# Performance work log

Hardware: AMD Instinct MI355X
Metric: run time of the kernel (lower is better)

Reference implementation:

```python
import jax, jax.numpy as jnp
import numpy as np

B, S, D, H, DFF, L = 32, 512, 512, 8, 2048, 3
DK = D // H
NEG = -1e32


def _ln(x, g, b):
    m = jnp.mean(x, axis=-1, keepdims=True)
    v = jnp.mean((x - m) ** 2, axis=-1, keepdims=True)
    return (x - m) / jnp.sqrt(v + 1e-5) * g + b


def _mha(query, key, value, mask, zero_pad, gam, Wk, bk, Wv, bv, Wo, bo):
    # kq_same: q and k both use k_linear
    q = (query @ Wk + bk).reshape(B, S, H, DK).transpose(0, 2, 1, 3)
    k = (key @ Wk + bk).reshape(B, S, H, DK).transpose(0, 2, 1, 3)
    v = (value @ Wv + bv).reshape(B, S, H, DK).transpose(0, 2, 1, 3)
    scores = jnp.einsum('bhid,bhjd->bhij', q, k) / jnp.sqrt(jnp.float32(DK))
    # distance-decay rescoring (no-grad in original)
    p = jax.nn.softmax(jnp.where(mask, scores, NEG), axis=-1) * mask
    distcum = jnp.cumsum(p, axis=-1)
    disttotal = jnp.sum(p, axis=-1, keepdims=True)
    idx = jnp.arange(S)
    pos = jnp.abs(idx[None, :] - idx[:, None]).astype(jnp.float32)  # [S,S]
    dist = jax.lax.stop_gradient(
        jnp.sqrt(jnp.clip((disttotal - distcum) * pos[None, None], 0.0, None)))
    gamma = -jax.nn.softplus(gam)[None, :, None, None]  # [1,H,1,1]
    total_effect = jnp.clip(jnp.exp(dist * gamma), 1e-5, 1e5)
    scores = jnp.where(mask, scores * total_effect, NEG)
    scores = jax.nn.softmax(scores, axis=-1)
    if zero_pad:
        scores = scores * (idx[:, None] > 0)[None, None, :, :].astype(scores.dtype) * 0 + \
                 scores * (idx > 0).astype(scores.dtype)[None, None, :, None]
    out = jnp.einsum('bhij,bhjd->bhid', scores, v)
    out = out.transpose(0, 2, 1, 3).reshape(B, S, D)
    return out @ Wo + bo


def _layer(i, mask, zero_pad, query, key, values, apply_pos,
           Wk, bk, Wv, bv, Wo, bo, gammas, ln1_g, ln1_b, W1, b1, W2, b2, ln2_g, ln2_b):
    a = _mha(query, key, values, mask, zero_pad, gammas[i],
             Wk[i], bk[i], Wv[i], bv[i], Wo[i], bo[i])
    x = _ln(query + a, ln1_g[i], ln1_b[i])
    if apply_pos:
        f = jax.nn.relu(x @ W1[i] + b1[i]) @ W2[i] + b2[i]
        x = _ln(x + f, ln2_g[i], ln2_b[i])
    return x


def setup_inputs() -> dict:
    key = jax.random.key(0)
    ks = jax.random.split(key, 12)
    sc = 0.02
    inp = {
        'q_embed_data': jax.random.normal(ks[0], (B, S, D), jnp.float32),
        'qa_embed_data': jax.random.normal(ks[1], (B, S, D), jnp.float32),
        'Wk': jax.random.normal(ks[2], (L, D, D), jnp.float32) * sc,
        'bk': jnp.zeros((L, D), jnp.float32),
        'Wv': jax.random.normal(ks[3], (L, D, D), jnp.float32) * sc,
        'bv': jnp.zeros((L, D), jnp.float32),
        'Wo': jax.random.normal(ks[4], (L, D, D), jnp.float32) * sc,
        'bo': jnp.zeros((L, D), jnp.float32),
        'gammas': jax.random.normal(ks[5], (L, H), jnp.float32) * 0.5,
        'ln1_g': jnp.ones((L, D), jnp.float32),
        'ln1_b': jnp.zeros((L, D), jnp.float32),
        'W1': jax.random.normal(ks[6], (L, D, DFF), jnp.float32) * sc,
        'b1': jnp.zeros((L, DFF), jnp.float32),
        'W2': jax.random.normal(ks[7], (L, DFF, D), jnp.float32) * sc,
        'b2': jnp.zeros((L, D), jnp.float32),
        'ln2_g': jnp.ones((L, D), jnp.float32),
        'ln2_b': jnp.zeros((L, D), jnp.float32),
    }
    return inp


def reference(q_embed_data, qa_embed_data, Wk, bk, Wv, bv, Wo, bo, gammas,
              ln1_g, ln1_b, W1, b1, W2, b2, ln2_g, ln2_b):
    P = (Wk, bk, Wv, bv, Wo, bo, gammas, ln1_g, ln1_b, W1, b1, W2, b2, ln2_g, ln2_b)
    mask1 = jnp.tril(jnp.ones((S, S), bool), 0)[None, None]   # peek current+past
    mask0 = jnp.tril(jnp.ones((S, S), bool), -1)[None, None]  # peek only past
    y = qa_embed_data
    x = q_embed_data
    # blocks_1 (n_blocks=1): mask=1, self-attn, apply_pos
    y = _layer(0, mask1, False, y, y, y, True, *P)
    # blocks_2 (2 layers): first mask=1 no FFN, second mask=0 zero_pad cross-attn to y
    x = _layer(1, mask1, False, x, x, x, False, *P)
    x = _layer(2, mask0, True, x, x, y, True, *P)
    return x
```

## Files before the change

kernel.cpp:

```cpp
#include <hip/hip_runtime.h>

#define BB   32
#define SS   512
#define DDIM 512
#define HH   8
#define DFFN 2048
#define MR   (BB*SS)

typedef unsigned int   u32;
typedef unsigned short u16;
typedef unsigned char  u8;
typedef __attribute__((ext_vector_type(8))) short bf16x8;
typedef __attribute__((ext_vector_type(4))) float f32x4;

__device__ __forceinline__ u32 packbf2(float x, float y) {
  u32 ux = __float_as_uint(x), uy = __float_as_uint(y);
  u32 hx = (ux + 0x7FFFu + ((ux >> 16) & 1u)) >> 16;
  u32 hy = (uy + 0x7FFFu + ((uy >> 16) & 1u)) >> 16;
  return hx | (hy << 16);
}
__device__ __forceinline__ u16 pack1bf(float x) {
  u32 u = __float_as_uint(x);
  return (u16)((u + 0x7FFFu + ((u >> 16) & 1u)) >> 16);
}
__device__ __forceinline__ float bf1(u16 h)  { return __uint_as_float(((u32)h) << 16); }

__device__ __forceinline__ float redsum2(float v) {
  v += __shfl_xor(v, 16, 64);
  v += __shfl_xor(v, 32, 64);
  return v;
}
__device__ __forceinline__ float redmax2(float v) {
  v = fmaxf(v, __shfl_xor(v, 16, 64));
  v = fmaxf(v, __shfl_xor(v, 32, 64));
  return v;
}

__global__ __launch_bounds__(256) void pack_flat(const float* __restrict__ in,
                                                 u16* __restrict__ out) {
  size_t i = ((size_t)blockIdx.x * 256 + threadIdx.x) * 8;
  float4 a = *(const float4*)(in + i);
  float4 b = *(const float4*)(in + i + 4);
  uint4 o;
  o.x = packbf2(a.x, a.y); o.y = packbf2(a.z, a.w);
  o.z = packbf2(b.x, b.y); o.w = packbf2(b.z, b.w);
  *(uint4*)(out + i) = o;
}

__global__ __launch_bounds__(256) void pack_w_t(const float* __restrict__ in,
                                                u16* __restrict__ out, int K, int N) {
  __shared__ float tile[64][65];
  const int t  = threadIdx.x;
  const int n0 = blockIdx.x * 64, k0 = blockIdx.y * 64;
  in  += (size_t)blockIdx.z * K * N;
  out += (size_t)blockIdx.z * N * K;
  #pragma unroll
  for (int it = 0; it < 4; ++it) {
    int idx = it * 256 + t;
    int kk = idx >> 4, n4 = idx & 15;
    float4 v = *(const float4*)(in + (size_t)(k0 + kk) * N + n0 + n4 * 4);
    tile[kk][n4*4+0] = v.x; tile[kk][n4*4+1] = v.y;
    tile[kk][n4*4+2] = v.z; tile[kk][n4*4+3] = v.w;
  }
  __syncthreads();
  #pragma unroll
  for (int it = 0; it < 4; ++it) {
    int idx = it * 256 + t;
    int nn = idx >> 4, g = idx & 15;
    uint2 o;
    o.x = packbf2(tile[g*4+0][nn], tile[g*4+1][nn]);
    o.y = packbf2(tile[g*4+2][nn], tile[g*4+3][nn]);
    *(uint2*)(out + (size_t)(n0 + nn) * K + k0 + g * 4) = o;
  }
}

__global__ __launch_bounds__(512, 2) void gemm8(
    const u16* __restrict__ Aa, const u16* __restrict__ Ab, int lda,
    const u16* __restrict__ Ba, const u16* __restrict__ Bb, int ldb,
    const float* __restrict__ biasa, const float* __restrict__ biasb,
    float* __restrict__ outFa, float* __restrict__ outFb,
    u16* __restrict__ outBa, u16* __restrict__ outBb,
    int ldc, int Kz, int relu)
{
  __shared__ __align__(16) u8 lds[131072];

  const int z = blockIdx.z;
  const u16* A    = z ? Ab : Aa;
  const u16* Bt   = z ? Bb : Ba;
  const float* bias = z ? biasb : biasa;
  float* outF = z ? outFb : outFa;
  u16*   outB = z ? outBb : outBa;

  const int nwg  = gridDim.x * gridDim.y;
  const int orig = blockIdx.y * gridDim.x + blockIdx.x;
  const int q8   = nwg >> 3, r8 = nwg & 7;
  const int xcd  = orig & 7, idx8 = orig >> 3;
  const int wg   = (xcd < r8 ? xcd * (q8 + 1) : r8 * (q8 + 1) + (xcd - r8) * q8) + idx8;
  const int bx   = wg % gridDim.x, by = wg / gridDim.x;
  const int row0 = by * 256, col0 = bx * 256;

  const int t    = threadIdx.x;
  const int lane = t & 63, wid = t >> 6;
  const int wm   = wid >> 2, wn = wid & 3;
  const int rl   = lane & 15, kg = lane >> 4;

  const int NT = Kz >> 6;

  f32x4 acc[8][4] = {};

  auto stageA = [&](int buf, int h, int kt) {
    #pragma unroll
    for (int l = 0; l < 2; ++l) {
      int s  = (l * 512 + t) >> 3;
      int kb = ((lane & 7) * 16) ^ ((s & 7) << 4);
      int row = row0 + ((s >> 6) * 128) + h * 64 + (s & 63);
      const u8* src = (const u8*)A + (size_t)row * lda * 2 + (size_t)kt * 128 + kb;
      u8* dst = lds + buf * 65536 + h * 16384 + (l * 512 + wid * 64) * 16;
      __builtin_amdgcn_global_load_lds(
          (const __attribute__((address_space(1))) u32*)src,
          (__attribute__((address_space(3))) u32*)dst, 16, 0, 0);
    }
  };
  auto stageB = [&](int buf, int h, int kt) {
    #pragma unroll
    for (int l = 0; l < 2; ++l) {
      int s  = (l * 512 + t) >> 3;
      int kb = ((lane & 7) * 16) ^ ((s & 7) << 4);
      int col = col0 + ((s >> 5) * 64) + h * 32 + (s & 31);
      const u8* src = (const u8*)Bt + (size_t)col * ldb * 2 + (size_t)kt * 128 + kb;
      u8* dst = lds + buf * 65536 + 32768 + h * 16384 + (l * 512 + wid * 64) * 16;
      __builtin_amdgcn_global_load_lds(
          (const __attribute__((address_space(1))) u32*)src,
          (__attribute__((address_space(3))) u32*)dst, 16, 0, 0);
    }
  };

  auto rdA = [&](int buf, int mh, int m, int ks) -> bf16x8 {
    int s = wm * 64 + m * 16 + rl;
    int off = buf * 65536 + mh * 16384 + s * 128 + (((ks * 32 + kg * 8) * 2) ^ ((s & 7) << 4));
    return *(const bf16x8*)(lds + off);
  };
  auto rdB = [&](int buf, int nh, int n, int ks) -> bf16x8 {
    int s = wn * 32 + n * 16 + rl;
    int off = buf * 65536 + 32768 + nh * 16384 + s * 128 + (((ks * 32 + kg * 8) * 2) ^ ((s & 7) << 4));
    return *(const bf16x8*)(lds + off);
  };

#define GBAR asm volatile("s_barrier" ::: "memory")
#define VMW4 asm volatile("s_waitcnt vmcnt(4)" ::: "memory")

#define PHASE(BUF, MH, NH, STAGECODE, DOVM) do {                               \
    bf16x8 af_[4][2], bf_[2][2];                                               \
    _Pragma("unroll") for (int m_ = 0; m_ < 4; ++m_)                           \
      _Pragma("unroll") for (int k_ = 0; k_ < 2; ++k_)                         \
        af_[m_][k_] = rdA(BUF, MH, m_, k_);                                    \
    _Pragma("unroll") for (int n_ = 0; n_ < 2; ++n_)                           \
      _Pragma("unroll") for (int k_ = 0; k_ < 2; ++k_)                         \
        bf_[n_][k_] = rdB(BUF, NH, n_, k_);                                    \
    STAGECODE;                                                                 \
    if (DOVM) VMW4;                                                            \
    GBAR;                                                                      \
    __builtin_amdgcn_s_setprio(1);                                             \
    _Pragma("unroll") for (int m_ = 0; m_ < 4; ++m_)                           \
      _Pragma("unroll") for (int n_ = 0; n_ < 2; ++n_) {                       \
        acc[(MH)*4+m_][(NH)*2+n_] = __builtin_amdgcn_mfma_f32_16x16x32_bf16(   \
            af_[m_][0], bf_[n_][0], acc[(MH)*4+m_][(NH)*2+n_], 0, 0, 0);       \
        acc[(MH)*4+m_][(NH)*2+n_] = __builtin_amdgcn_mfma_f32_16x16x32_bf16(   \
            af_[m_][1], bf_[n_][1], acc[(MH)*4+m_][(NH)*2+n_], 0, 0, 0);       \
      }                                                                        \
    __builtin_amdgcn_s_setprio(0);                                             \
    GBAR;                                                                      \
  } while (0)

  stageA(0, 0, 0); stageB(0, 0, 0); stageA(0, 1, 0); stageB(0, 1, 0);
  stageA(1, 0, 1); stageB(1, 0, 1);
  VMW4; GBAR;

  for (int i = 0; i < (NT >> 1); ++i) {
    const int T1 = 2 * i + 1;
    int T2 = 2 * i + 2; if (T2 >= NT) T2 -= NT;
    int T3 = 2 * i + 3; if (T3 >= NT) T3 -= NT;
    PHASE(0, 0, 0, stageA(1, 1, T1), 0);
    PHASE(0, 0, 1, stageB(1, 1, T1), 0);
    PHASE(0, 1, 0, stageA(0, 0, T2), 0);
    PHASE(0, 1, 1, stageB(0, 0, T2), 1);
    PHASE(1, 0, 0, stageA(0, 1, T2), 0);
    PHASE(1, 0, 1, stageB(0, 1, T2), 0);
    PHASE(1, 1, 0, stageA(1, 0, T3), 0);
    PHASE(1, 1, 1, stageB(1, 0, T3), 1);
  }
#undef PHASE
#undef GBAR
#undef VMW4

  #pragma unroll
  for (int M = 0; M < 8; ++M) {
    #pragma unroll
    for (int N2 = 0; N2 < 4; ++N2) {
      const int col = col0 + wn * 64 + N2 * 16 + rl;
      const float bs = bias ? bias[col] : 0.f;
      #pragma unroll
      for (int q = 0; q < 4; ++q) {
        const int row = row0 + wm * 128 + M * 16 + kg * 4 + q;
        float v = acc[M][N2][q] + bs;
        if (relu) v = fmaxf(v, 0.f);
        if (outF) outF[(size_t)row * ldc + col] = v;
        if (outB) outB[(size_t)row * ldc + col] = pack1bf(v);
      }
    }
  }
}

__global__ __attribute__((amdgpu_flat_work_group_size(512, 512)))
           __attribute__((amdgpu_waves_per_eu(1, 2)))
void attn_mfma(
    const u16* __restrict__ qk, const u16* __restrict__ vbuf,
    const float* __restrict__ gam, u16* __restrict__ out,
    int mask_excl, int zero_pad)
{
  __shared__ __align__(16) u8 kSb[65536];
  __shared__ __align__(16) u8 vTb[65536];
  __shared__ __align__(16) u8 pChb[8192];

  const int t    = threadIdx.x;
  const int lane = t & 63, wid = t >> 6;
  const int ql   = lane & 15, g = lane >> 4;
  const int bh   = blockIdx.x, b = bh >> 3, h = bh & 7;
  const size_t base = (size_t)b * SS * DDIM + (size_t)h * 64;

  float gv = gam[h];
  float sp = (gv > 0.f) ? (gv + log1pf(__expf(-gv))) : log1pf(__expf(gv));
  const float gamma = -sp;

  for (int it = 0; it < 8; ++it) {
    int idx = it * 512 + t;
    int j = idx >> 3, u = idx & 7;
    uint4 w = *(const uint4*)(qk + base + (size_t)j * DDIM + u * 8);
    *(uint4*)(kSb + ((j * 128 + u * 16) ^ ((j & 7) << 4))) = w;
  }
  for (int it = 0; it < 8; ++it) {
    int idx = it * 512 + t;
    int j = idx >> 3, u = idx & 7;
    union { uint4 v4; u16 s[8]; } uu;
    uu.v4 = *(const uint4*)(vbuf + base + (size_t)j * DDIM + u * 8);
    #pragma unroll
    for (int dd = 0; dd < 8; ++dd) {
      int d = u * 8 + dd;
      *(u16*)(vTb + d * 1024 + ((2 * j) ^ ((dd ^ u) << 4))) = uu.s[dd];
    }
  }
  __syncthreads();

  bool vm[4];
  #pragma unroll
  for (int rg = 0; rg < 4; ++rg) {
    int kl = 4 * g + rg;
    vm[rg] = mask_excl ? (kl < ql) : (kl <= ql);
  }

  u8* pB = pChb + wid * 1024;
  const int swp = (ql & 3) << 4;

  int vbase[4], vsw[4];
  #pragma unroll
  for (int n = 0; n < 4; ++n) {
    int d = n * 16 + ql;
    vbase[n] = d * 1024;
    vsw[n]   = ((d & 7) ^ ((d >> 3) & 7)) << 4;
  }

  #pragma unroll
  for (int ri = 0; ri < 4; ++ri) {
    int r0_ = (ri == 0) ? wid : (ri == 1) ? (15 - wid) : (ri == 2) ? (16 + wid) : (31 - wid);
    const int rs = __builtin_amdgcn_readfirstlane(r0_);
    const int i0 = rs * 16;

    const int qrow = i0 + ql;
    const int qsw  = (qrow & 7) << 4;
    bf16x8 qf0 = *(const bf16x8*)(kSb + ((qrow * 128      + g * 16) ^ qsw));
    bf16x8 qf1 = *(const bf16x8*)(kSb + ((qrow * 128 + 64 + g * 16) ^ qsw));

    float mrun = -3.0e38f, Srun = 0.f;
    #pragma unroll
    for (int kt = 0; kt < 32; ++kt) {
      if (kt <= rs) {
        const bool dg = (kt == rs);
        const int krow = kt * 16 + ql;
        const int ksw  = (krow & 7) << 4;
        bf16x8 ka0 = *(const bf16x8*)(kSb + ((krow * 128      + g * 16) ^ ksw));
        bf16x8 ka1 = *(const bf16x8*)(kSb + ((krow * 128 + 64 + g * 16) ^ ksw));
        f32x4 dv = {};
        dv = __builtin_amdgcn_mfma_f32_16x16x32_bf16(ka0, qf0, dv, 0, 0, 0);
        dv = __builtin_amdgcn_mfma_f32_16x16x32_bf16(ka1, qf1, dv, 0, 0, 0);
        float s0 = dv[0] * 0.125f, s1 = dv[1] * 0.125f;
        float s2 = dv[2] * 0.125f, s3 = dv[3] * 0.125f;
        const bool v0 = !dg || vm[0], v1 = !dg || vm[1];
        const bool v2 = !dg || vm[2], v3 = !dg || vm[3];
        float kmax = fmaxf(fmaxf(v0 ? s0 : -3.0e38f, v1 ? s1 : -3.0e38f),
                           fmaxf(v2 ? s2 : -3.0e38f, v3 ? s3 : -3.0e38f));
        float nm = fmaxf(mrun, kmax);
        Srun *= __expf(mrun - nm);
        float e0 = v0 ? __expf(s0 - nm) : 0.f;
        float e1 = v1 ? __expf(s1 - nm) : 0.f;
        float e2 = v2 ? __expf(s2 - nm) : 0.f;
        float e3 = v3 ? __expf(s3 - nm) : 0.f;
        Srun += (e0 + e1) + (e2 + e3);
        mrun = nm;
      }
    }
    const float m1 = redmax2(mrun);
    const float S1 = redsum2(Srun * __expf(mrun - m1));
    const float inv1 = (S1 > 0.f) ? (1.f / S1) : 0.f;
    const float M2p  = fmaxf(m1, 0.f);

    f32x4 oacc[4] = {};
    float cbase = 0.f, S2l = 0.f;
    const float qlf = (float)(i0 + ql);

    auto subkt = [&](int kt, bool dg, u32& wA, u32& wB) {
      const int krow = kt * 16 + ql;
      const int ksw  = (krow & 7) << 4;
      bf16x8 ka0 = *(const bf16x8*)(kSb + ((krow * 128      + g * 16) ^ ksw));
      bf16x8 ka1 = *(const bf16x8*)(kSb + ((krow * 128 + 64 + g * 16) ^ ksw));
      f32x4 dv = {};
      dv = __builtin_amdgcn_mfma_f32_16x16x32_bf16(ka0, qf0, dv, 0, 0, 0);
      dv = __builtin_amdgcn_mfma_f32_16x16x32_bf16(ka1, qf1, dv, 0, 0, 0);
      float sv[4];
      sv[0] = dv[0] * 0.125f; sv[1] = dv[1] * 0.125f;
      sv[2] = dv[2] * 0.125f; sv[3] = dv[3] * 0.125f;
      const bool v0 = !dg || vm[0], v1 = !dg || vm[1];
      const bool v2 = !dg || vm[2], v3 = !dg || vm[3];
      float e0 = v0 ? __expf(sv[0] - m1) : 0.f;
      float e1 = v1 ? __expf(sv[1] - m1) : 0.f;
      float e2 = v2 ? __expf(sv[2] - m1) : 0.f;
      float e3 = v3 ? __expf(sv[3] - m1) : 0.f;
      float p0 = e0, p1 = p0 + e1, p2 = p1 + e2, p3 = p2 + e3;
      float a16 = __shfl_up(p3, 16, 64);
      float a32 = __shfl_up(p3, 32, 64);
      float a48 = __shfl_up(p3, 48, 64);
      float gp = (g >= 1 ? a16 : 0.f) + (g >= 2 ? a32 : 0.f) + (g >= 3 ? a48 : 0.f);
      float tt = __shfl(gp + p3, ql + 48, 64);
      const float pbase = cbase + gp;
      const float pf = qlf - (float)(kt * 16 + 4 * g);
      float ipr[4] = {p0, p1, p2, p3};
      bool  vv[4]  = {v0, v1, v2, v3};
      float q2[4];
      #pragma unroll
      for (int rg = 0; rg < 4; ++rg) {
        float rem  = fmaxf((S1 - (pbase + ipr[rg])) * inv1, 0.f);
        float pos  = pf - (float)rg;
        float dist = sqrtf(fmaxf(rem * pos, 0.f));
        float eff  = fmaxf(__expf(gamma * dist), 1e-5f);
        float s2v  = sv[rg] * eff;
        float ee   = vv[rg] ? __expf(s2v - M2p) : 0.f;
        q2[rg] = ee;
        S2l += ee;
      }
      wA = packbf2(q2[0], q2[1]);
      wB = packbf2(q2[2], q2[3]);
      cbase += tt;
    };

    #pragma unroll
    for (int c = 0; c < 16; ++c) {
      if (2 * c <= rs) {
        u32 w0 = 0, w1 = 0, w2 = 0, w3 = 0;
        subkt(2 * c, (2 * c == rs), w0, w1);
        if (2 * c + 1 <= rs) subkt(2 * c + 1, (2 * c + 1 == rs), w2, w3);
        *(u32*)(pB + ((ql * 64 +      8 * g    ) ^ swp)) = w0;
        *(u32*)(pB + ((ql * 64 +      8 * g + 4) ^ swp)) = w1;
        *(u32*)(pB + ((ql * 64 + 32 + 8 * g    ) ^ swp)) = w2;
        *(u32*)(pB + ((ql * 64 + 32 + 8 * g + 4) ^ swp)) = w3;
        bf16x8 pa = *(const bf16x8*)(pB + ((ql * 64 + 16 * g) ^ swp));
        #pragma unroll
        for (int n = 0; n < 4; ++n) {
          bf16x8 vb = *(const bf16x8*)(vTb + vbase[n] + ((64 * c + 16 * g) ^ vsw[n]));
          oacc[n] = __builtin_amdgcn_mfma_f32_16x16x32_bf16(pa, vb, oacc[n], 0, 0, 0);
        }
      }
    }

    const float S2   = redsum2(S2l);
    const float inv2 = 1.f / fmaxf(S2, 1e-30f);
    float i2[4];
    #pragma unroll
    for (int rg = 0; rg < 4; ++rg) i2[rg] = __shfl(inv2, 4 * g + rg, 64);

    #pragma unroll
    for (int n = 0; n < 4; ++n) {
      #pragma unroll
      for (int rg = 0; rg < 4; ++rg) {
        const int qo = i0 + 4 * g + rg;
        float val = oacc[n][rg] * i2[rg];
        if (zero_pad && qo == 0) val = 0.f;
        out[base + (size_t)qo * DDIM + n * 16 + ql] = pack1bf(val);
      }
    }
  }
}

__global__ __launch_bounds__(256) void ln_kernel(
    const float* __restrict__ a, const float* __restrict__ bsrc,
    const float* __restrict__ csrc,
    const float* __restrict__ g, const float* __restrict__ be,
    float* __restrict__ outF, u16* __restrict__ outB)
{
  const int lane = threadIdx.x & 63, w = threadIdx.x >> 6;
  const size_t row = (size_t)blockIdx.x * 4 + w;
  const float* pa = a    + row * DDIM;
  const float* pb = bsrc + row * DDIM;
  const float* pc = csrc ? csrc + row * DDIM : nullptr;
  float v[8];
  float sum = 0.f;
  #pragma unroll
  for (int c = 0; c < 2; ++c) {
    float4 va = *(const float4*)(pa + c * 256 + lane * 4);
    float4 vb = *(const float4*)(pb + c * 256 + lane * 4);
    v[c*4+0] = va.x + vb.x; v[c*4+1] = va.y + vb.y;
    v[c*4+2] = va.z + vb.z; v[c*4+3] = va.w + vb.w;
    if (pc) {
      float4 vc = *(const float4*)(pc + c * 256 + lane * 4);
      v[c*4+0] += vc.x; v[c*4+1] += vc.y; v[c*4+2] += vc.z; v[c*4+3] += vc.w;
    }
    sum += v[c*4+0] + v[c*4+1] + v[c*4+2] + v[c*4+3];
  }
  #pragma unroll
  for (int off = 32; off > 0; off >>= 1) sum += __shfl_xor(sum, off, 64);
  const float mean = sum * (1.f / 512.f);
  float var = 0.f;
  #pragma unroll
  for (int k = 0; k < 8; ++k) { float dd = v[k] - mean; var = fmaf(dd, dd, var); }
  #pragma unroll
  for (int off = 32; off > 0; off >>= 1) var += __shfl_xor(var, off, 64);
  var *= (1.f / 512.f);
  const float inv = rsqrtf(var + 1e-5f);
  #pragma unroll
  for (int c = 0; c < 2; ++c) {
    float4 gg = *(const float4*)(g  + c * 256 + lane * 4);
    float4 bb = *(const float4*)(be + c * 256 + lane * 4);
    float4 o;
    o.x = (v[c*4+0] - mean) * inv * gg.x + bb.x;
    o.y = (v[c*4+1] - mean) * inv * gg.y + bb.y;
    o.z = (v[c*4+2] - mean) * inv * gg.z + bb.z;
    o.w = (v[c*4+3] - mean) * inv * gg.w + bb.w;
    const size_t off4 = row * DDIM + c * 256 + lane * 4;
    if (outF) *(float4*)(outF + off4) = o;
    if (outB) {
      uint2 p;
      p.x = packbf2(o.x, o.y); p.y = packbf2(o.z, o.w);
      *(uint2*)(outB + off4) = p;
    }
  }
}

extern "C" void kernel_launch(void* const* d_in, const int* in_sizes, int n_in,
                              void* d_out, int out_size, void* d_ws, size_t ws_size,
                              hipStream_t stream) {
  const float* qe  = (const float*)d_in[0];
  const float* qa  = (const float*)d_in[1];
  const float* Wk  = (const float*)d_in[2];
  const float* bk  = (const float*)d_in[3];
  const float* Wv  = (const float*)d_in[4];
  const float* bv  = (const float*)d_in[5];
  const float* Wo  = (const float*)d_in[6];
  const float* bo  = (const float*)d_in[7];
  const float* gm  = (const float*)d_in[8];
  const float* l1g = (const float*)d_in[9];
  const float* l1b = (const float*)d_in[10];
  const float* W1  = (const float*)d_in[11];
  const float* b1  = (const float*)d_in[12];
  const float* W2  = (const float*)d_in[13];
  const float* b2  = (const float*)d_in[14];
  const float* l2g = (const float*)d_in[15];
  const float* l2b = (const float*)d_in[16];

  char* ws = (char*)d_ws;
  u16* WT = (u16*)ws;
  u16* A0 = (u16*)(ws + ((size_t)18  << 20));
  u16* A1 = (u16*)(ws + ((size_t)34  << 20));
  u16* A2 = (u16*)(ws + ((size_t)50  << 20));
  u16* A3 = (u16*)(ws + ((size_t)66  << 20));
  float* F0 = (float*)(ws + ((size_t)82  << 20));
  float* F1 = (float*)(ws + ((size_t)114 << 20));
  u16* Amid = (u16*)(ws + ((size_t)146 << 20));
  float* PWo = (float*)Amid;
  float* PW2 = (float*)A2;

  u16* WkT = WT;
  u16* WvT = WT + (size_t)3 * 262144;
  u16* WoT = WT + (size_t)6 * 262144;
  u16* W1T = WT + (size_t)9 * 262144;
  u16* W2T = W1T + (size_t)3 * 1048576;

  pack_w_t<<<dim3(8, 8, 3),  256, 0, stream>>>(Wk, WkT, 512, 512);
  pack_w_t<<<dim3(8, 8, 3),  256, 0, stream>>>(Wv, WvT, 512, 512);
  pack_w_t<<<dim3(8, 8, 3),  256, 0, stream>>>(Wo, WoT, 512, 512);
  pack_w_t<<<dim3(32, 8, 3), 256, 0, stream>>>(W1, W1T, 512, 2048);
  pack_w_t<<<dim3(8, 32, 3), 256, 0, stream>>>(W2, W2T, 2048, 512);
  pack_flat<<<4096, 256, 0, stream>>>(qa, A0);
  pack_flat<<<4096, 256, 0, stream>>>(qe, A1);

  auto g8 = [&](const u16* Aa, const u16* Ab, int lda,
                const u16* Ba, const u16* Bb, int ldb,
                const float* ba, const float* bb,
                float* oFa, float* oFb, u16* oBa, u16* oBb,
                int ldc, int M, int N, int Kz, int relu, int nz) {
    gemm8<<<dim3(N / 256, M / 256, nz), 512, 0, stream>>>(
        Aa, Ab, lda, Ba, Bb, ldb, ba, bb, oFa, oFb, oBa, oBb, ldc, Kz, relu);
  };

  auto layer = [&](int li, const u16* qbf, const float* qf32, const u16* vbf,
                   int excl, int zp, int pos,
                   float* lnF, u16* lnB, float* y2F, u16* y2B) {
    const float* bk_l = bk + (size_t)li * DDIM;
    const float* bv_l = bv + (size_t)li * DDIM;
    const float* bo_l = bo + (size_t)li * DDIM;
    const float* gm_l = gm + (size_t)li * HH;
    const float* g1   = l1g + (size_t)li * DDIM;
    const float* be1  = l1b + (size_t)li * DDIM;
    const float* g2   = l2g + (size_t)li * DDIM;
    const float* be2  = l2b + (size_t)li * DDIM;
    const float* b1_l = b1 + (size_t)li * DFFN;
    const float* b2_l = b2 + (size_t)li * DDIM;
    const u16* WkT_l = WkT + (size_t)li * 262144;
    const u16* WvT_l = WvT + (size_t)li * 262144;
    const u16* WoT_l = WoT + (size_t)li * 262144;
    const u16* W1T_l = W1T + (size_t)li * 1048576;
    const u16* W2T_l = W2T + (size_t)li * 1048576;

    g8(qbf, vbf, 512, WkT_l, WvT_l, 512, bk_l, bv_l,
       nullptr, nullptr, A2, A3, 512, MR, 512, 512, 0, 2);
    attn_mfma<<<BB * HH, 512, 0, stream>>>(A2, A3, gm_l, A3, excl, zp);
    g8(A3, A3 + 256, 512, WoT_l, WoT_l + 256, 512, bo_l, nullptr,
       F0, PWo, nullptr, nullptr, 512, MR, 512, 256, 0, 2);
    ln_kernel<<<MR / 4, 256, 0, stream>>>(qf32, F0, PWo, g1, be1, lnF, lnB);
    if (pos) {
      g8(lnB, nullptr, 512, W1T_l, nullptr, 512, b1_l, nullptr,
         nullptr, nullptr, Amid, nullptr, 2048, MR, 2048, 512, 1, 1);
      g8(Amid, Amid + 1024, 2048, W2T_l, W2T_l + 1024, 2048, b2_l, nullptr,
         F0, PW2, nullptr, nullptr, 512, MR, 512, 1024, 0, 2);
      ln_kernel<<<MR / 4, 256, 0, stream>>>(lnF, F0, PW2, g2, be2, y2F, y2B);
    }
  };

  layer(0, A0, qa, A0, 0, 0, 1, F1, A2, nullptr, A0);
  layer(1, A1, qe, A1, 0, 0, 0, F1, A1, nullptr, nullptr);
  layer(2, A1, F1, A0, 1, 1, 1, F1, A1, (float*)d_out, nullptr);
}
```

Before: 742.2 us.

## Split attention across two blocks per head with pre-transposed V in global memory

Adds a separate vt_pack kernel that writes V transposed per (batch, head) into a workspace buffer. The attention kernel then reads V fragments straight from global/L2 instead of staging a 64KB transposed copy in LDS, which halves its LDS use and allows two blocks per CU. The grid doubles so each block handles half of the query tiles (two row-tiles per wave instead of four), keeping the balanced causal pairing. The online max-tracked softmax is replaced by a clamped exponent without max subtraction, which removes work and shuffles but relies on the scores staying small enough not to overflow.

```diff
diff --git a/kernel.cpp b/kernel.cpp
--- a/kernel.cpp
+++ b/kernel.cpp
@@ -23,18 +23,14 @@
   u32 u = __float_as_uint(x);
   return (u16)((u + 0x7FFFu + ((u >> 16) & 1u)) >> 16);
 }
-__device__ __forceinline__ float bf1(u16 h)  { return __uint_as_float(((u32)h) << 16); }
 
 __device__ __forceinline__ float redsum2(float v) {
   v += __shfl_xor(v, 16, 64);
   v += __shfl_xor(v, 32, 64);
   return v;
 }
-__device__ __forceinline__ float redmax2(float v) {
-  v = fmaxf(v, __shfl_xor(v, 16, 64));
-  v = fmaxf(v, __shfl_xor(v, 32, 64));
-  return v;
-}
+
+__device__ __forceinline__ float expc(float x) { return __expf(fminf(x, 80.f)); }
 
 __global__ __launch_bounds__(256) void pack_flat(const float* __restrict__ in,
                                                  u16* __restrict__ out) {
@@ -71,6 +67,33 @@
     o.x = packbf2(tile[g*4+0][nn], tile[g*4+1][nn]);
     o.y = packbf2(tile[g*4+2][nn], tile[g*4+3][nn]);
     *(uint2*)(out + (size_t)(n0 + nn) * K + k0 + g * 4) = o;
+  }
+}
+
+__global__ __launch_bounds__(256) void vt_pack(const u16* __restrict__ v,
+                                               u16* __restrict__ vt) {
+  __shared__ u16 tile[128][72];
+  const int t  = threadIdx.x;
+  const int bh = blockIdx.x, b = bh >> 3, h = bh & 7;
+  const int s0 = blockIdx.y * 128;
+  const u16* src = v + (size_t)b * SS * DDIM + (size_t)h * 64;
+  #pragma unroll
+  for (int it = 0; it < 4; ++it) {
+    int id = it * 256 + t;
+    int si = id >> 3, dseg = id & 7;
+    uint4 w = *(const uint4*)(src + (size_t)(s0 + si) * DDIM + dseg * 8);
+    *(uint4*)&tile[si][dseg * 8] = w;
+  }
+  __syncthreads();
+  u16* dst = vt + (size_t)bh * 64 * SS + s0;
+  #pragma unroll
+  for (int it = 0; it < 4; ++it) {
+    int id = it * 256 + t;
+    int d = id >> 4, sc = id & 15;
+    u16 buf[8];
+    #pragma unroll
+    for (int j = 0; j < 8; ++j) buf[j] = tile[sc * 8 + j][d];
+    *(uint4*)(dst + (size_t)d * SS + sc * 8) = *(uint4*)buf;
   }
 }
 
@@ -211,22 +234,21 @@
   }
 }
 
-__global__ __attribute__((amdgpu_flat_work_group_size(512, 512)))
-           __attribute__((amdgpu_waves_per_eu(1, 2)))
-void attn_mfma(
-    const u16* __restrict__ qk, const u16* __restrict__ vbuf,
+__global__ __launch_bounds__(512, 2) void attn_mfma(
+    const u16* __restrict__ qk, const u16* __restrict__ vt,
     const float* __restrict__ gam, u16* __restrict__ out,
     int mask_excl, int zero_pad)
 {
   __shared__ __align__(16) u8 kSb[65536];
-  __shared__ __align__(16) u8 vTb[65536];
   __shared__ __align__(16) u8 pChb[8192];
 
   const int t    = threadIdx.x;
   const int lane = t & 63, wid = t >> 6;
   const int ql   = lane & 15, g = lane >> 4;
-  const int bh   = blockIdx.x, b = bh >> 3, h = bh & 7;
+  const int bh   = blockIdx.x >> 1, z = blockIdx.x & 1;
+  const int b    = bh >> 3, h = bh & 7;
   const size_t base = (size_t)b * SS * DDIM + (size_t)h * 64;
+  const u16* vtb = vt + (size_t)bh * 64 * SS;
 
   float gv = gam[h];
   float sp = (gv > 0.f) ? (gv + log1pf(__expf(-gv))) : log1pf(__expf(gv));
@@ -238,17 +260,6 @@
     uint4 w = *(const uint4*)(qk + base + (size_t)j * DDIM + u * 8);
     *(uint4*)(kSb + ((j * 128 + u * 16) ^ ((j & 7) << 4))) = w;
   }
-  for (int it = 0; it < 8; ++it) {
-    int idx = it * 512 + t;
-    int j = idx >> 3, u = idx & 7;
-    union { uint4 v4; u16 s[8]; } uu;
-    uu.v4 = *(const uint4*)(vbuf + base + (size_t)j * DDIM + u * 8);
-    #pragma unroll
-    for (int dd = 0; dd < 8; ++dd) {
-      int d = u * 8 + dd;
-      *(u16*)(vTb + d * 1024 + ((2 * j) ^ ((dd ^ u) << 4))) = uu.s[dd];
-    }
-  }
   __syncthreads();
 
   bool vm[4];
@@ -261,18 +272,10 @@
   u8* pB = pChb + wid * 1024;
   const int swp = (ql & 3) << 4;
 
-  int vbase[4], vsw[4];
-  #pragma unroll
-  for (int n = 0; n < 4; ++n) {
-    int d = n * 16 + ql;
-    vbase[n] = d * 1024;
-    vsw[n]   = ((d & 7) ^ ((d >> 3) & 7)) << 4;
-  }
-
-  #pragma unroll
-  for (int ri = 0; ri < 4; ++ri) {
-    int r0_ = (ri == 0) ? wid : (ri == 1) ? (15 - wid) : (ri == 2) ? (16 + wid) : (31 - wid);
-    const int rs = __builtin_amdgcn_readfirstlane(r0_);
+  #pragma unroll
+  for (int ri = 0; ri < 2; ++ri) {
+    const int v_ = z * 8 + wid;
+    const int rs = __builtin_amdgcn_readfirstlane(ri ? (31 - v_) : v_);
     const int i0 = rs * 16;
 
     const int qrow = i0 + ql;
@@ -280,7 +283,7 @@
     bf16x8 qf0 = *(const bf16x8*)(kSb + ((qrow * 128      + g * 16) ^ qsw));
     bf16x8 qf1 = *(const bf16x8*)(kSb + ((qrow * 128 + 64 + g * 16) ^ qsw));
 
-    float mrun = -3.0e38f, Srun = 0.f;
+    float S1l = 0.f;
     #pragma unroll
     for (int kt = 0; kt < 32; ++kt) {
       if (kt <= rs) {
@@ -292,26 +295,15 @@
         f32x4 dv = {};
         dv = __builtin_amdgcn_mfma_f32_16x16x32_bf16(ka0, qf0, dv, 0, 0, 0);
         dv = __builtin_amdgcn_mfma_f32_16x16x32_bf16(ka1, qf1, dv, 0, 0, 0);
-        float s0 = dv[0] * 0.125f, s1 = dv[1] * 0.125f;
-        float s2 = dv[2] * 0.125f, s3 = dv[3] * 0.125f;
-        const bool v0 = !dg || vm[0], v1 = !dg || vm[1];
-        const bool v2 = !dg || vm[2], v3 = !dg || vm[3];
-        float kmax = fmaxf(fmaxf(v0 ? s0 : -3.0e38f, v1 ? s1 : -3.0e38f),
-                           fmaxf(v2 ? s2 : -3.0e38f, v3 ? s3 : -3.0e38f));
-        float nm = fmaxf(mrun, kmax);
-        Srun *= __expf(mrun - nm);
-        float e0 = v0 ? __expf(s0 - nm) : 0.f;
-        float e1 = v1 ? __expf(s1 - nm) : 0.f;
-        float e2 = v2 ? __expf(s2 - nm) : 0.f;
-        float e3 = v3 ? __expf(s3 - nm) : 0.f;
-        Srun += (e0 + e1) + (e2 + e3);
-        mrun = nm;
+        float e0 = (!dg || vm[0]) ? expc(dv[0] * 0.125f) : 0.f;
+        float e1 = (!dg || vm[1]) ? expc(dv[1] * 0.125f) : 0.f;
+        float e2 = (!dg || vm[2]) ? expc(dv[2] * 0.125f) : 0.f;
+        float e3 = (!dg || vm[3]) ? expc(dv[3] * 0.125f) : 0.f;
+        S1l += (e0 + e1) + (e2 + e3);
       }
     }
-    const float m1 = redmax2(mrun);
-    const float S1 = redsum2(Srun * __expf(mrun - m1));
+    const float S1   = redsum2(S1l);
     const float inv1 = (S1 > 0.f) ? (1.f / S1) : 0.f;
-    const float M2p  = fmaxf(m1, 0.f);
 
     f32x4 oacc[4] = {};
     float cbase = 0.f, S2l = 0.f;
@@ -330,10 +322,10 @@
       sv[2] = dv[2] * 0.125f; sv[3] = dv[3] * 0.125f;
       const bool v0 = !dg || vm[0], v1 = !dg || vm[1];
       const bool v2 = !dg || vm[2], v3 = !dg || vm[3];
-      float e0 = v0 ? __expf(sv[0] - m1) : 0.f;
-      float e1 = v1 ? __expf(sv[1] - m1) : 0.f;
-      float e2 = v2 ? __expf(sv[2] - m1) : 0.f;
-      float e3 = v3 ? __expf(sv[3] - m1) : 0.f;
+      float e0 = v0 ? expc(sv[0]) : 0.f;
+      float e1 = v1 ? expc(sv[1]) : 0.f;
+      float e2 = v2 ? expc(sv[2]) : 0.f;
+      float e3 = v3 ? expc(sv[3]) : 0.f;
       float p0 = e0, p1 = p0 + e1, p2 = p1 + e2, p3 = p2 + e3;
       float a16 = __shfl_up(p3, 16, 64);
       float a32 = __shfl_up(p3, 32, 64);
@@ -351,8 +343,7 @@
         float pos  = pf - (float)rg;
         float dist = sqrtf(fmaxf(rem * pos, 0.f));
         float eff  = fmaxf(__expf(gamma * dist), 1e-5f);
-        float s2v  = sv[rg] * eff;
-        float ee   = vv[rg] ? __expf(s2v - M2p) : 0.f;
+        float ee   = vv[rg] ? expc(sv[rg] * eff) : 0.f;
         q2[rg] = ee;
         S2l += ee;
       }
@@ -374,7 +365,7 @@
         bf16x8 pa = *(const bf16x8*)(pB + ((ql * 64 + 16 * g) ^ swp));
         #pragma unroll
         for (int n = 0; n < 4; ++n) {
-          bf16x8 vb = *(const bf16x8*)(vTb + vbase[n] + ((64 * c + 16 * g) ^ vsw[n]));
+          bf16x8 vb = *(const bf16x8*)(vtb + (size_t)(n * 16 + ql) * SS + 32 * c + 8 * g);
           oacc[n] = __builtin_amdgcn_mfma_f32_16x16x32_bf16(pa, vb, oacc[n], 0, 0, 0);
         }
       }
@@ -485,6 +476,7 @@
   u16* Amid = (u16*)(ws + ((size_t)146 << 20));
   float* PWo = (float*)Amid;
   float* PW2 = (float*)A2;
+  u16* VT   = (u16*)F0;
 
   u16* WkT = WT;
   u16* WvT = WT + (size_t)3 * 262144;
@@ -530,7 +522,8 @@
 
     g8(qbf, vbf, 512, WkT_l, WvT_l, 512, bk_l, bv_l,
        nullptr, nullptr, A2, A3, 512, MR, 512, 512, 0, 2);
-    attn_mfma<<<BB * HH, 512, 0, stream>>>(A2, A3, gm_l, A3, excl, zp);
+    vt_pack<<<dim3(BB * HH, 4), 256, 0, stream>>>(A3, VT);
+    attn_mfma<<<BB * HH * 2, 512, 0, stream>>>(A2, VT, gm_l, A3, excl, zp);
     g8(A3, A3 + 256, 512, WoT_l, WoT_l + 256, 512, bo_l, nullptr,
        F0, PWo, nullptr, nullptr, 512, MR, 512, 256, 0, 2);
     ln_kernel<<<MR / 4, 256, 0, stream>>>(qf32, F0, PWo, g1, be1, lnF, lnB);
```

Result: slower. 829.3 us (+11.7%).

## Drop softmax max-subtraction, fold score scale into QK GEMM, read residual in bf16

Applied to the files above, without the earlier changes.

The 1/sqrt(dk) scale moves into the K projection GEMM epilogue as sqrt of the scale on both q and k. The attention kernel then drops the running-max online softmax and uses clamped exponentials (exp(min(x,80))) directly, removing the max reduction and rescaling work. LayerNorm now reads the residual input as bf16 instead of fp32, which removes fp32 residual buffers and some traffic. The LDS swizzle for the P chunk also changes. Skipping the max subtraction relies on scores being small enough not to overflow, and the bf16 residual loses precision.

```diff
diff --git a/kernel.cpp b/kernel.cpp
--- a/kernel.cpp
+++ b/kernel.cpp
@@ -23,18 +23,14 @@
   u32 u = __float_as_uint(x);
   return (u16)((u + 0x7FFFu + ((u >> 16) & 1u)) >> 16);
 }
-__device__ __forceinline__ float bf1(u16 h)  { return __uint_as_float(((u32)h) << 16); }
 
 __device__ __forceinline__ float redsum2(float v) {
   v += __shfl_xor(v, 16, 64);
   v += __shfl_xor(v, 32, 64);
   return v;
 }
-__device__ __forceinline__ float redmax2(float v) {
-  v = fmaxf(v, __shfl_xor(v, 16, 64));
-  v = fmaxf(v, __shfl_xor(v, 32, 64));
-  return v;
-}
+
+__device__ __forceinline__ float expc(float x) { return __expf(fminf(x, 80.f)); }
 
 __global__ __launch_bounds__(256) void pack_flat(const float* __restrict__ in,
                                                  u16* __restrict__ out) {
@@ -80,7 +76,7 @@
     const float* __restrict__ biasa, const float* __restrict__ biasb,
     float* __restrict__ outFa, float* __restrict__ outFb,
     u16* __restrict__ outBa, u16* __restrict__ outBb,
-    int ldc, int Kz, int relu)
+    int ldc, int Kz, int relu, float sca, float scb)
 {
   __shared__ __align__(16) u8 lds[131072];
 
@@ -90,6 +86,7 @@
   const float* bias = z ? biasb : biasa;
   float* outF = z ? outFb : outFa;
   u16*   outB = z ? outBb : outBa;
+  const float sc = z ? scb : sca;
 
   const int nwg  = gridDim.x * gridDim.y;
   const int orig = blockIdx.y * gridDim.x + blockIdx.x;
@@ -202,7 +199,7 @@
       #pragma unroll
       for (int q = 0; q < 4; ++q) {
         const int row = row0 + wm * 128 + M * 16 + kg * 4 + q;
-        float v = acc[M][N2][q] + bs;
+        float v = (acc[M][N2][q] + bs) * sc;
         if (relu) v = fmaxf(v, 0.f);
         if (outF) outF[(size_t)row * ldc + col] = v;
         if (outB) outB[(size_t)row * ldc + col] = pack1bf(v);
@@ -259,7 +256,7 @@
   }
 
   u8* pB = pChb + wid * 1024;
-  const int swp = (ql & 3) << 4;
+  const int swp = (ql & 7) << 4;
 
   int vbase[4], vsw[4];
   #pragma unroll
@@ -280,7 +277,7 @@
     bf16x8 qf0 = *(const bf16x8*)(kSb + ((qrow * 128      + g * 16) ^ qsw));
     bf16x8 qf1 = *(const bf16x8*)(kSb + ((qrow * 128 + 64 + g * 16) ^ qsw));
 
-    float mrun = -3.0e38f, Srun = 0.f;
+    float S1l = 0.f;
     #pragma unroll
     for (int kt = 0; kt < 32; ++kt) {
       if (kt <= rs) {
@@ -292,26 +289,15 @@
         f32x4 dv = {};
         dv = __builtin_amdgcn_mfma_f32_16x16x32_bf16(ka0, qf0, dv, 0, 0, 0);
         dv = __builtin_amdgcn_mfma_f32_16x16x32_bf16(ka1, qf1, dv, 0, 0, 0);
-        float s0 = dv[0] * 0.125f, s1 = dv[1] * 0.125f;
-        float s2 = dv[2] * 0.125f, s3 = dv[3] * 0.125f;
-        const bool v0 = !dg || vm[0], v1 = !dg || vm[1];
-        const bool v2 = !dg || vm[2], v3 = !dg || vm[3];
-        float kmax = fmaxf(fmaxf(v0 ? s0 : -3.0e38f, v1 ? s1 : -3.0e38f),
-                           fmaxf(v2 ? s2 : -3.0e38f, v3 ? s3 : -3.0e38f));
-        float nm = fmaxf(mrun, kmax);
-        Srun *= __expf(mrun - nm);
-        float e0 = v0 ? __expf(s0 - nm) : 0.f;
-        float e1 = v1 ? __expf(s1 - nm) : 0.f;
-        float e2 = v2 ? __expf(s2 - nm) : 0.f;
-        float e3 = v3 ? __expf(s3 - nm) : 0.f;
-        Srun += (e0 + e1) + (e2 + e3);
-        mrun = nm;
+        float e0 = (!dg || vm[0]) ? expc(dv[0]) : 0.f;
+        float e1 = (!dg || vm[1]) ? expc(dv[1]) : 0.f;
+        float e2 = (!dg || vm[2]) ? expc(dv[2]) : 0.f;
+        float e3 = (!dg || vm[3]) ? expc(dv[3]) : 0.f;
+        S1l += (e0 + e1) + (e2 + e3);
       }
     }
-    const float m1 = redmax2(mrun);
-    const float S1 = redsum2(Srun * __expf(mrun - m1));
+    const float S1   = redsum2(S1l);
     const float inv1 = (S1 > 0.f) ? (1.f / S1) : 0.f;
-    const float M2p  = fmaxf(m1, 0.f);
 
     f32x4 oacc[4] = {};
     float cbase = 0.f, S2l = 0.f;
@@ -325,15 +311,12 @@
       f32x4 dv = {};
       dv = __builtin_amdgcn_mfma_f32_16x16x32_bf16(ka0, qf0, dv, 0, 0, 0);
       dv = __builtin_amdgcn_mfma_f32_16x16x32_bf16(ka1, qf1, dv, 0, 0, 0);
-      float sv[4];
-      sv[0] = dv[0] * 0.125f; sv[1] = dv[1] * 0.125f;
-      sv[2] = dv[2] * 0.125f; sv[3] = dv[3] * 0.125f;
       const bool v0 = !dg || vm[0], v1 = !dg || vm[1];
       const bool v2 = !dg || vm[2], v3 = !dg || vm[3];
-      float e0 = v0 ? __expf(sv[0] - m1) : 0.f;
-      float e1 = v1 ? __expf(sv[1] - m1) : 0.f;
-      float e2 = v2 ? __expf(sv[2] - m1) : 0.f;
-      float e3 = v3 ? __expf(sv[3] - m1) : 0.f;
+      float e0 = v0 ? expc(dv[0]) : 0.f;
+      float e1 = v1 ? expc(dv[1]) : 0.f;
+      float e2 = v2 ? expc(dv[2]) : 0.f;
+      float e3 = v3 ? expc(dv[3]) : 0.f;
       float p0 = e0, p1 = p0 + e1, p2 = p1 + e2, p3 = p2 + e3;
       float a16 = __shfl_up(p3, 16, 64);
       float a32 = __shfl_up(p3, 32, 64);
@@ -344,6 +327,7 @@
       const float pf = qlf - (float)(kt * 16 + 4 * g);
       float ipr[4] = {p0, p1, p2, p3};
       bool  vv[4]  = {v0, v1, v2, v3};
+      float sv[4]  = {dv[0], dv[1], dv[2], dv[3]};
       float q2[4];
       #pragma unroll
       for (int rg = 0; rg < 4; ++rg) {
@@ -351,8 +335,7 @@
         float pos  = pf - (float)rg;
         float dist = sqrtf(fmaxf(rem * pos, 0.f));
         float eff  = fmaxf(__expf(gamma * dist), 1e-5f);
-        float s2v  = sv[rg] * eff;
-        float ee   = vv[rg] ? __expf(s2v - M2p) : 0.f;
+        float ee   = vv[rg] ? expc(sv[rg] * eff) : 0.f;
         q2[rg] = ee;
         S2l += ee;
       }
@@ -400,30 +383,35 @@
 }
 
 __global__ __launch_bounds__(256) void ln_kernel(
-    const float* __restrict__ a, const float* __restrict__ bsrc,
+    const u16* __restrict__ a, const float* __restrict__ bsrc,
     const float* __restrict__ csrc,
     const float* __restrict__ g, const float* __restrict__ be,
     float* __restrict__ outF, u16* __restrict__ outB)
 {
   const int lane = threadIdx.x & 63, w = threadIdx.x >> 6;
   const size_t row = (size_t)blockIdx.x * 4 + w;
-  const float* pa = a    + row * DDIM;
-  const float* pb = bsrc + row * DDIM;
-  const float* pc = csrc ? csrc + row * DDIM : nullptr;
+  const size_t off8 = row * DDIM + lane * 8;
+
+  uint4 ab = *(const uint4*)(a + off8);
+  const u16* ap = (const u16*)&ab;
   float v[8];
+  #pragma unroll
+  for (int k = 0; k < 8; ++k) v[k] = __uint_as_float(((u32)ap[k]) << 16);
+
+  float4 b0 = *(const float4*)(bsrc + off8);
+  float4 b1 = *(const float4*)(bsrc + off8 + 4);
+  v[0] += b0.x; v[1] += b0.y; v[2] += b0.z; v[3] += b0.w;
+  v[4] += b1.x; v[5] += b1.y; v[6] += b1.z; v[7] += b1.w;
+  if (csrc) {
+    float4 c0 = *(const float4*)(csrc + off8);
+    float4 c1 = *(const float4*)(csrc + off8 + 4);
+    v[0] += c0.x; v[1] += c0.y; v[2] += c0.z; v[3] += c0.w;
+    v[4] += c1.x; v[5] += c1.y; v[6] += c1.z; v[7] += c1.w;
+  }
+
   float sum = 0.f;
   #pragma unroll
-  for (int c = 0; c < 2; ++c) {
-    float4 va = *(const float4*)(pa + c * 256 + lane * 4);
-    float4 vb = *(const float4*)(pb + c * 256 + lane * 4);
-    v[c*4+0] = va.x + vb.x; v[c*4+1] = va.y + vb.y;
-    v[c*4+2] = va.z + vb.z; v[c*4+3] = va.w + vb.w;
-    if (pc) {
-      float4 vc = *(const float4*)(pc + c * 256 + lane * 4);
-      v[c*4+0] += vc.x; v[c*4+1] += vc.y; v[c*4+2] += vc.z; v[c*4+3] += vc.w;
-    }
-    sum += v[c*4+0] + v[c*4+1] + v[c*4+2] + v[c*4+3];
-  }
+  for (int k = 0; k < 8; ++k) sum += v[k];
   #pragma unroll
   for (int off = 32; off > 0; off >>= 1) sum += __shfl_xor(sum, off, 64);
   const float mean = sum * (1.f / 512.f);
@@ -434,22 +422,28 @@
   for (int off = 32; off > 0; off >>= 1) var += __shfl_xor(var, off, 64);
   var *= (1.f / 512.f);
   const float inv = rsqrtf(var + 1e-5f);
-  #pragma unroll
-  for (int c = 0; c < 2; ++c) {
-    float4 gg = *(const float4*)(g  + c * 256 + lane * 4);
-    float4 bb = *(const float4*)(be + c * 256 + lane * 4);
-    float4 o;
-    o.x = (v[c*4+0] - mean) * inv * gg.x + bb.x;
-    o.y = (v[c*4+1] - mean) * inv * gg.y + bb.y;
-    o.z = (v[c*4+2] - mean) * inv * gg.z + bb.z;
-    o.w = (v[c*4+3] - mean) * inv * gg.w + bb.w;
-    const size_t off4 = row * DDIM + c * 256 + lane * 4;
-    if (outF) *(float4*)(outF + off4) = o;
-    if (outB) {
-      uint2 p;
-      p.x = packbf2(o.x, o.y); p.y = packbf2(o.z, o.w);
-      *(uint2*)(outB + off4) = p;
-    }
+
+  float4 g0 = *(const float4*)(g + lane * 8);
+  float4 g1 = *(const float4*)(g + lane * 8 + 4);
+  float4 e0 = *(const float4*)(be + lane * 8);
+  float4 e1 = *(const float4*)(be + lane * 8 + 4);
+  float gv[8] = {g0.x, g0.y, g0.z, g0.w, g1.x, g1.y, g1.z, g1.w};
+  float ev[8] = {e0.x, e0.y, e0.z, e0.w, e1.x, e1.y, e1.z, e1.w};
+  float o[8];
+  #pragma unroll
+  for (int k = 0; k < 8; ++k) o[k] = (v[k] - mean) * inv * gv[k] + ev[k];
+
+  if (outF) {
+    float4 f0 = {o[0], o[1], o[2], o[3]};
+    float4 f1 = {o[4], o[5], o[6], o[7]};
+    *(float4*)(outF + off8)     = f0;
+    *(float4*)(outF + off8 + 4) = f1;
+  }
+  if (outB) {
+    uint4 p;
+    p.x = packbf2(o[0], o[1]); p.y = packbf2(o[2], o[3]);
+    p.z = packbf2(o[4], o[5]); p.w = packbf2(o[6], o[7]);
+    *(uint4*)(outB + off8) = p;
   }
 }
 
@@ -481,10 +475,9 @@
   u16* A2 = (u16*)(ws + ((size_t)50  << 20));
   u16* A3 = (u16*)(ws + ((size_t)66  << 20));
   float* F0 = (float*)(ws + ((size_t)82  << 20));
-  float* F1 = (float*)(ws + ((size_t)114 << 20));
+  float* PW2 = (float*)(ws + ((size_t)114 << 20));
   u16* Amid = (u16*)(ws + ((size_t)146 << 20));
   float* PWo = (float*)Amid;
-  float* PW2 = (float*)A2;
 
   u16* WkT = WT;
   u16* WvT = WT + (size_t)3 * 262144;
@@ -500,18 +493,22 @@
   pack_flat<<<4096, 256, 0, stream>>>(qa, A0);
   pack_flat<<<4096, 256, 0, stream>>>(qe, A1);
 
+  const float SQ = 0.35355339059327373f;
+
   auto g8 = [&](const u16* Aa, const u16* Ab, int lda,
                 const u16* Ba, const u16* Bb, int ldb,
                 const float* ba, const float* bb,
                 float* oFa, float* oFb, u16* oBa, u16* oBb,
-                int ldc, int M, int N, int Kz, int relu, int nz) {
+                int ldc, int M, int N, int Kz, int relu, int nz,
+                float sca, float scb) {
     gemm8<<<dim3(N / 256, M / 256, nz), 512, 0, stream>>>(
-        Aa, Ab, lda, Ba, Bb, ldb, ba, bb, oFa, oFb, oBa, oBb, ldc, Kz, relu);
+        Aa, Ab, lda, Ba, Bb, ldb, ba, bb, oFa, oFb, oBa, oBb, ldc, Kz, relu,
+        sca, scb);
   };
 
-  auto layer = [&](int li, const u16* qbf, const float* qf32, const u16* vbf,
+  auto layer = [&](int li, const u16* qbf, const u16* vbf,
                    int excl, int zp, int pos,
-                   float* lnF, u16* lnB, float* y2F, u16* y2B) {
+                   u16* x1B, u16* y2B, float* y2F) {
     const float* bk_l = bk + (size_t)li * DDIM;
     const float* bv_l = bv + (size_t)li * DDIM;
     const float* bo_l = bo + (size_t)li * DDIM;
@@ -529,21 +526,21 @@
     const u16* W2T_l = W2T + (size_t)li * 1048576;
 
     g8(qbf, vbf, 512, WkT_l, WvT_l, 512, bk_l, bv_l,
-       nullptr, nullptr, A2, A3, 512, MR, 512, 512, 0, 2);
+       nullptr, nullptr, A2, A3, 512, MR, 512, 512, 0, 2, SQ, 1.f);
     attn_mfma<<<BB * HH, 512, 0, stream>>>(A2, A3, gm_l, A3, excl, zp);
     g8(A3, A3 + 256, 512, WoT_l, WoT_l + 256, 512, bo_l, nullptr,
-       F0, PWo, nullptr, nullptr, 512, MR, 512, 256, 0, 2);
-    ln_kernel<<<MR / 4, 256, 0, stream>>>(qf32, F0, PWo, g1, be1, lnF, lnB);
+       F0, PWo, nullptr, nullptr, 512, MR, 512, 256, 0, 2, 1.f, 1.f);
+    ln_kernel<<<MR / 4, 256, 0, stream>>>(qbf, F0, PWo, g1, be1, nullptr, x1B);
     if (pos) {
-      g8(lnB, nullptr, 512, W1T_l, nullptr, 512, b1_l, nullptr,
-         nullptr, nullptr, Amid, nullptr, 2048, MR, 2048, 512, 1, 1);
+      g8(x1B, nullptr, 512, W1T_l, nullptr, 512, b1_l, nullptr,
+         nullptr, nullptr, Amid, nullptr, 2048, MR, 2048, 512, 1, 1, 1.f, 1.f);
       g8(Amid, Amid + 1024, 2048, W2T_l, W2T_l + 1024, 2048, b2_l, nullptr,
-         F0, PW2, nullptr, nullptr, 512, MR, 512, 1024, 0, 2);
-      ln_kernel<<<MR / 4, 256, 0, stream>>>(lnF, F0, PW2, g2, be2, y2F, y2B);
+         F0, PW2, nullptr, nullptr, 512, MR, 512, 1024, 0, 2, 1.f, 1.f);
+      ln_kernel<<<MR / 4, 256, 0, stream>>>(x1B, F0, PW2, g2, be2, y2F, y2B);
     }
   };
 
-  layer(0, A0, qa, A0, 0, 0, 1, F1, A2, nullptr, A0);
-  layer(1, A1, qe, A1, 0, 0, 0, F1, A1, nullptr, nullptr);
-  layer(2, A1, F1, A0, 1, 1, 1, F1, A1, (float*)d_out, nullptr);
-}
+  layer(0, A0, A0, 0, 0, 1, A2, A0, nullptr);
+  layer(1, A1, A1, 0, 0, 0, A1, nullptr, nullptr);
+  layer(2, A1, A0, 1, 1, 1, A1, nullptr, (float*)d_out);
+}
```

Measured after the change: 700.0 us. -5.7%, faster.
